# Optimization experiments

Measured on AMD Instinct MI355X. Metric: run time of the kernel, lower is better.

The kernel has to match this reference:

```python
import jax, jax.numpy as jnp
import numpy as np

N_NODES = 100000
N_EDGES = 1600000
D = 128
L = 2


def setup_inputs() -> dict:
    key = jax.random.key(0)
    ks = jax.random.split(key, 8)
    s = 1.0 / np.sqrt(D)
    return {
        "x": jax.random.normal(ks[0], (N_NODES, D), dtype=jnp.float32),
        "edge_index": jax.random.randint(ks[1], (2, N_EDGES), 0, N_NODES, dtype=jnp.int64),
        "edge_weight": jax.random.uniform(ks[2], (N_EDGES,), dtype=jnp.float32),
        "weight": jax.random.normal(ks[3], (L, D, D), dtype=jnp.float32) * s,
        "w_ih": jax.random.normal(ks[4], (3 * D, D), dtype=jnp.float32) * s,
        "w_hh": jax.random.normal(ks[5], (3 * D, D), dtype=jnp.float32) * s,
        "b_ih": jax.random.normal(ks[6], (3 * D,), dtype=jnp.float32) * s,
        "b_hh": jax.random.normal(ks[7], (3 * D,), dtype=jnp.float32) * s,
    }


def _gru_cell(m, h, w_ih, w_hh, b_ih, b_hh):
    # torch.nn.GRUCell: gates ordered (reset, update, new)
    gi = m @ w_ih.T + b_ih  # [N, 3D]
    gh = h @ w_hh.T + b_hh  # [N, 3D]
    i_r, i_z, i_n = jnp.split(gi, 3, axis=-1)
    h_r, h_z, h_n = jnp.split(gh, 3, axis=-1)
    r = jax.nn.sigmoid(i_r + h_r)
    z = jax.nn.sigmoid(i_z + h_z)
    n = jnp.tanh(i_n + r * h_n)
    return (1.0 - z) * n + z * h


def reference(x, edge_index, edge_weight, weight, w_ih, w_hh, b_ih, b_hh):
    src = edge_index[0]
    dst = edge_index[1]
    h = x  # in_channels == out_channels, no zero-padding needed
    for i in range(L):
        m = h @ weight[i]                          # [N, D]
        msg = m[src] * edge_weight[:, None]        # [E, D] gather + scale
        agg = jax.ops.segment_sum(msg, dst, num_segments=N_NODES)  # scatter-add
        h = _gru_cell(agg, h, w_ih, w_hh, b_ih, b_hh)
    return h
```

## Files before the change

kernel.cpp:

```cpp
#include <hip/hip_runtime.h>
#include <hip/hip_bf16.h>
#include <stdint.h>

typedef unsigned short u16;
typedef unsigned long long u64;
typedef __attribute__((ext_vector_type(8))) short bf16x8;
typedef __attribute__((ext_vector_type(4))) float f32x4;

#define DD 128
#define NB 256
#define SB 10240

__device__ __forceinline__ u16 f2bf(float f){
  uint32_t u = __float_as_uint(f);
  uint32_t r = (u + 0x7fffu + ((u >> 16) & 1u)) >> 16;
  return (u16)r;
}
__device__ __forceinline__ float bf2f(u16 h){ return __uint_as_float(((uint32_t)h) << 16); }

struct Frag2 { bf16x8 hi, lo; };

__device__ __forceinline__ Frag2 split8(float4 v0, float4 v1){
  union { float f[8]; uint32_t u[8]; } U;
  *(float4*)&U.f[0] = v0; *(float4*)&U.f[4] = v1;
  union { uint32_t w[4]; bf16x8 v; } H, L;
  #pragma unroll
  for (int q = 0; q < 4; q++){
    uint32_t a = U.u[2*q], b = U.u[2*q+1];
    H.w[q] = __builtin_amdgcn_perm(b, a, 0x07060302);
    float l0 = U.f[2*q]   - __uint_as_float(a & 0xffff0000u);
    float l1 = U.f[2*q+1] - __uint_as_float(b & 0xffff0000u);
    L.w[q] = __builtin_amdgcn_perm(__float_as_uint(l1), __float_as_uint(l0), 0x07060302);
  }
  Frag2 r; r.hi = H.v; r.lo = L.v; return r;
}

__device__ __forceinline__ Frag2 load_afrag_g(const float* A, int row, int k0){
  const float4* p = (const float4*)(A + (size_t)row * DD + k0);
  return split8(p[0], p[1]);
}

__global__ void pack_kernel(const float* __restrict__ whh, const float* __restrict__ bih,
                            const float* __restrict__ bhh, u16* __restrict__ hhb,
                            float* __restrict__ bias, int* __restrict__ gcursor){
  int tid = blockIdx.x * 256 + threadIdx.x;
  int lane = tid & 63;
  int b1 = 6144, b2 = b1 + 512, b3 = b2 + NB;
  if (tid < b1){
    int kc = (tid >> 6) & 3, t = tid >> 8;
    int row = t*16 + (lane & 15), kb = kc*32 + 8*(lane >> 4);
    #pragma unroll
    for (int e = 0; e < 8; e++)
      hhb[(size_t)tid*8 + e] = f2bf(whh[(size_t)row*DD + kb + e]);
  } else if (tid < b2){
    int id = tid - b1;
    if (id < 256)      bias[id] = bih[id] + bhh[id];
    else if (id < 384) bias[id] = bih[id];
    else               bias[id] = bhh[id - 128];
  } else if (tid < b3){
    gcursor[tid - b2] = 0;
  }
}

__global__ __launch_bounds__(256) void wc_kernel(const float* __restrict__ w,
    const float* __restrict__ wih, u16* __restrict__ wcb, int L){
  int tid = blockIdx.x*256 + threadIdx.x;
  if (tid >= L*49152) return;
  int l = tid / 49152;
  int r = tid % 49152;
  int k = r / 384;
  int g = r % 384;
  const float4* wr = (const float4*)(w + (size_t)l*DD*DD + (size_t)k*DD);
  const float4* ir = (const float4*)(wih + (size_t)g*DD);
  float acc = 0.f;
  #pragma unroll
  for (int j = 0; j < 32; j++){
    float4 a = wr[j], b = ir[j];
    acc += a.x*b.x + a.y*b.y + a.z*b.z + a.w*b.w;
  }
  int gate = g >> 7, c = g & 127;
  int jt = c >> 4, lrow = c & 15;
  int kc = k >> 5, sub = (k >> 3) & 3, e = k & 7;
  wcb[(size_t)l*49152 + (size_t)(((gate*8 + jt)*4 + kc)*512 + (sub*16 + lrow)*8 + e)]
      = f2bf(acc);
}

__global__ void conv_kernel(const float* __restrict__ x, u16* __restrict__ hb, int n4){
  int i = blockIdx.x*256 + threadIdx.x;
  if (i < n4){
    float4 v = ((const float4*)x)[i];
    ushort4 o;
    o.x = f2bf(v.x); o.y = f2bf(v.y); o.z = f2bf(v.z); o.w = f2bf(v.w);
    ((ushort4*)hb)[i] = o;
  }
}

__global__ __launch_bounds__(256) void binA_kernel(const int* __restrict__ src,
    const int* __restrict__ dst, const float* __restrict__ ew,
    int* __restrict__ gcursor, u64* __restrict__ staging, int E, int N){
  __shared__ unsigned lcnt[NB];
  __shared__ unsigned lbase[NB];
  __shared__ unsigned lcur[NB];
  __shared__ unsigned gbase[NB];
  __shared__ unsigned char sbucket[4096];
  __shared__ u64 sedge[4096];
  const int CH = 4096;
  int tid = threadIdx.x;
  int e0 = blockIdx.x * CH;

  lcnt[tid] = 0;
  __syncthreads();
  for (int i = tid; i < CH; i += 256){
    int e = e0 + i;
    if (e < E){
      unsigned d = (unsigned)dst[e];
      if (d < (unsigned)N) atomicAdd(&lcnt[d >> 9], 1u);
    }
  }
  __syncthreads();
  lbase[tid] = lcnt[tid];
  __syncthreads();
  for (int off = 1; off < NB; off <<= 1){
    unsigned t = (tid >= off) ? lbase[tid - off] : 0u;
    __syncthreads();
    lbase[tid] += t;
    __syncthreads();
  }
  unsigned total = lbase[NB - 1];
  lbase[tid] -= lcnt[tid];
  gbase[tid] = (unsigned)atomicAdd(&gcursor[tid], (int)lcnt[tid]);
  lcur[tid] = lbase[tid];
  __syncthreads();
  for (int i = tid; i < CH; i += 256){
    int e = e0 + i;
    if (e < E){
      unsigned d = (unsigned)dst[e];
      if (d < (unsigned)N){
        unsigned b = d >> 9;
        unsigned p = atomicAdd(&lcur[b], 1u);
        unsigned s = (unsigned)src[e];
        sedge[p] = ((u64)__float_as_uint(ew[e]) << 32) | ((u64)(s & 0x1FFFFu) << 9)
                 | (u64)(d & 0x1FFu);
        sbucket[p] = (unsigned char)b;
      }
    }
  }
  __syncthreads();
  for (int i = tid; i < (int)total; i += 256){
    unsigned b = sbucket[i];
    unsigned gpos = gbase[b] + ((unsigned)i - lbase[b]);
    if (gpos < SB) staging[(size_t)b*SB + gpos] = sedge[i];
  }
}

__global__ __launch_bounds__(256) void binB_kernel(const u64* __restrict__ staging,
    const int* __restrict__ gcursor, int* __restrict__ row_ptr,
    uint2* __restrict__ entries, int N, int E){
  __shared__ int sg[NB];
  __shared__ unsigned ncnt[512];
  __shared__ unsigned nsc[512];
  __shared__ unsigned ncur[512];
  int tid = threadIdx.x;
  int b = blockIdx.x;
  sg[tid] = gcursor[tid];
  __syncthreads();
  for (int off = 1; off < NB; off <<= 1){
    int t = (tid >= off) ? sg[tid - off] : 0;
    __syncthreads();
    sg[tid] += t;
    __syncthreads();
  }
  int cnt = gcursor[b];
  if (cnt > SB) cnt = SB;
  int base = sg[b] - cnt;
  if (b == NB - 1 && tid == 0) row_ptr[N] = sg[NB - 1];
  const u64* st = staging + (size_t)b * SB;

  ncnt[tid] = 0; ncnt[tid + 256] = 0;
  __syncthreads();
  for (int i = tid; i < cnt; i += 256)
    atomicAdd(&ncnt[(unsigned)(st[i] & 0x1FFu)], 1u);
  __syncthreads();
  nsc[tid] = ncnt[tid]; nsc[tid + 256] = ncnt[tid + 256];
  __syncthreads();
  for (int off = 1; off < 512; off <<= 1){
    unsigned t0 = (tid >= off) ? nsc[tid - off] : 0u;
    unsigned t1 = (tid + 256 >= off) ? nsc[tid + 256 - off] : 0u;
    __syncthreads();
    nsc[tid] += t0; nsc[tid + 256] += t1;
    __syncthreads();
  }
  #pragma unroll
  for (int h = 0; h < 2; h++){
    int k = tid + h*256;
    unsigned excl = nsc[k] - ncnt[k];
    int g = b*512 + k;
    if (g < N) row_ptr[g] = base + (int)excl;
    ncur[k] = excl;
  }
  __syncthreads();
  for (int i = tid; i < cnt; i += 256){
    u64 v = st[i];
    unsigned local = (unsigned)(v & 0x1FFu);
    unsigned p = atomicAdd(&ncur[local], 1u);
    uint2 ent;
    ent.x = (unsigned)((v >> 9) & 0x1FFFFu);
    ent.y = (unsigned)(v >> 32);
    entries[base + p] = ent;
  }
}

__global__ __launch_bounds__(256) void gather_kernel(const int* __restrict__ row_ptr,
    const uint2* __restrict__ entries, const u16* __restrict__ hb,
    float* __restrict__ agg, int N){
  int lane = threadIdx.x & 63;
  int q = lane >> 4;
  int t = lane & 15;
  int node = (blockIdx.x*256 + threadIdx.x) >> 6;
  if (node >= N) return;
  int s = row_ptr[node], e = row_ptr[node + 1];
  float acc[8];
  #pragma unroll
  for (int c = 0; c < 8; c++) acc[c] = 0.f;
  #pragma unroll 4
  for (int i = s; i < e; i += 4){
    int idx = i + q;
    bool valid = idx < e;
    uint2 en = entries[valid ? idx : i];
    float w = valid ? __uint_as_float(en.y) : 0.f;
    uint4 mv = *(const uint4*)(hb + (size_t)en.x*DD + 8*t);
    acc[0] += w * __uint_as_float(mv.x << 16);
    acc[1] += w * __uint_as_float(mv.x & 0xffff0000u);
    acc[2] += w * __uint_as_float(mv.y << 16);
    acc[3] += w * __uint_as_float(mv.y & 0xffff0000u);
    acc[4] += w * __uint_as_float(mv.z << 16);
    acc[5] += w * __uint_as_float(mv.z & 0xffff0000u);
    acc[6] += w * __uint_as_float(mv.w << 16);
    acc[7] += w * __uint_as_float(mv.w & 0xffff0000u);
  }
  #pragma unroll
  for (int c = 0; c < 8; c++){
    acc[c] += __shfl_xor(acc[c], 16);
    acc[c] += __shfl_xor(acc[c], 32);
  }
  if (q == 0){
    float4 o0 = {acc[0], acc[1], acc[2], acc[3]};
    float4 o1 = {acc[4], acc[5], acc[6], acc[7]};
    *(float4*)(agg + (size_t)node*DD + 8*t)     = o0;
    *(float4*)(agg + (size_t)node*DD + 8*t + 4) = o1;
  }
}

__global__ __launch_bounds__(256, 4) void gru_kernel(
    const float* __restrict__ agg, const float* hin,
    const u16* __restrict__ wcb, const u16* __restrict__ hhb,
    const float* __restrict__ bias, float* hout, u16* hbout, int nstripes){
  __shared__ u16 lw[2][12*512];
  int lane = threadIdx.x & 63;
  int wid = threadIdx.x >> 6;
  int stripe = blockIdx.x*4 + wid;
  bool active = stripe < nstripes;
  int n0 = (active ? stripe : (nstripes - 1)) * 16;
  int lrow = lane & 15, lk = lane >> 4;

  Frag2 aa[4], ahf[4];
  #pragma unroll
  for (int kc = 0; kc < 4; kc++){
    int k0 = kc*32 + 8*lk;
    aa[kc]  = load_afrag_g(agg, n0 + lrow, k0);
    ahf[kc] = load_afrag_g(hin, n0 + lrow, k0);
  }

  int q = wid*3;
  int g0 = q >> 2,       kc0 = q & 3;
  int g1 = (q+1) >> 2,   kc1 = (q+1) & 3;
  int g2 = (q+2) >> 2,   kc2 = (q+2) & 3;

  {
    bf16x8 s0 = *(const bf16x8*)(wcb + ((size_t)((g0*8 + 0)*4 + kc0)*64 + lane)*8);
    bf16x8 s1 = *(const bf16x8*)(wcb + ((size_t)((g1*8 + 0)*4 + kc1)*64 + lane)*8);
    bf16x8 s2 = *(const bf16x8*)(wcb + ((size_t)((g2*8 + 0)*4 + kc2)*64 + lane)*8);
    *(bf16x8*)(lw[0] + ((size_t)(q+0)*64 + lane)*8) = s0;
    *(bf16x8*)(lw[0] + ((size_t)(q+1)*64 + lane)*8) = s1;
    *(bf16x8*)(lw[0] + ((size_t)(q+2)*64 + lane)*8) = s2;
  }
  __syncthreads();

  f32x4 zero = {0.f, 0.f, 0.f, 0.f};
  f32x4 ir = zero, iz = zero, in_ = zero, hr = zero, hz = zero, hn = zero;
  for (int ph = 0; ph < 16; ph++){
    int jt = ph >> 1, half = ph & 1;
    bf16x8 n0r, n1r, n2r;
    if (ph < 15){
      int njt = (ph + 1) >> 1;
      const u16* wsrc = ((ph + 1) & 1) ? hhb : wcb;
      n0r = *(const bf16x8*)(wsrc + ((size_t)((g0*8 + njt)*4 + kc0)*64 + lane)*8);
      n1r = *(const bf16x8*)(wsrc + ((size_t)((g1*8 + njt)*4 + kc1)*64 + lane)*8);
      n2r = *(const bf16x8*)(wsrc + ((size_t)((g2*8 + njt)*4 + kc2)*64 + lane)*8);
    }
    const u16* buf = lw[ph & 1];
    if (half == 0){
      ir = zero; iz = zero; in_ = zero;
      #pragma unroll
      for (int kc = 0; kc < 4; kc++){
        bf16x8 b0 = *(const bf16x8*)(buf + ((size_t)(0*4 + kc)*64 + lane)*8);
        bf16x8 b1 = *(const bf16x8*)(buf + ((size_t)(1*4 + kc)*64 + lane)*8);
        bf16x8 b2 = *(const bf16x8*)(buf + ((size_t)(2*4 + kc)*64 + lane)*8);
        ir  = __builtin_amdgcn_mfma_f32_16x16x32_bf16(aa[kc].hi, b0, ir,  0, 0, 0);
        ir  = __builtin_amdgcn_mfma_f32_16x16x32_bf16(aa[kc].lo, b0, ir,  0, 0, 0);
        iz  = __builtin_amdgcn_mfma_f32_16x16x32_bf16(aa[kc].hi, b1, iz,  0, 0, 0);
        iz  = __builtin_amdgcn_mfma_f32_16x16x32_bf16(aa[kc].lo, b1, iz,  0, 0, 0);
        in_ = __builtin_amdgcn_mfma_f32_16x16x32_bf16(aa[kc].hi, b2, in_, 0, 0, 0);
        in_ = __builtin_amdgcn_mfma_f32_16x16x32_bf16(aa[kc].lo, b2, in_, 0, 0, 0);
      }
    } else {
      hr = zero; hz = zero; hn = zero;
      #pragma unroll
      for (int kc = 0; kc < 4; kc++){
        bf16x8 b0 = *(const bf16x8*)(buf + ((size_t)(0*4 + kc)*64 + lane)*8);
        bf16x8 b1 = *(const bf16x8*)(buf + ((size_t)(1*4 + kc)*64 + lane)*8);
        bf16x8 b2 = *(const bf16x8*)(buf + ((size_t)(2*4 + kc)*64 + lane)*8);
        hr = __builtin_amdgcn_mfma_f32_16x16x32_bf16(ahf[kc].hi, b0, hr, 0, 0, 0);
        hr = __builtin_amdgcn_mfma_f32_16x16x32_bf16(ahf[kc].lo, b0, hr, 0, 0, 0);
        hz = __builtin_amdgcn_mfma_f32_16x16x32_bf16(ahf[kc].hi, b1, hz, 0, 0, 0);
        hz = __builtin_amdgcn_mfma_f32_16x16x32_bf16(ahf[kc].lo, b1, hz, 0, 0, 0);
        hn = __builtin_amdgcn_mfma_f32_16x16x32_bf16(ahf[kc].hi, b2, hn, 0, 0, 0);
        hn = __builtin_amdgcn_mfma_f32_16x16x32_bf16(ahf[kc].lo, b2, hn, 0, 0, 0);
      }
      if (active){
        int j = jt*16 + lrow;
        float br = bias[j];
        float bz = bias[128 + j];
        float bi = bias[256 + j];
        float bh = bias[384 + j];
        #pragma unroll
        for (int r = 0; r < 4; r++){
          int node = n0 + lk*4 + r;
          float xr = ir[r] + hr[r] + br;
          float xz = iz[r] + hz[r] + bz;
          float rg = __builtin_amdgcn_rcpf(1.f + __expf(-xr));
          float zg = __builtin_amdgcn_rcpf(1.f + __expf(-xz));
          float xn = in_[r] + bi + rg*(hn[r] + bh);
          xn = fminf(fmaxf(xn, -30.f), 30.f);
          float e2 = __expf(2.f*xn);
          float ng = 1.f - 2.f*__builtin_amdgcn_rcpf(e2 + 1.f);
          float hv = hin[(size_t)node*DD + j];
          float val = ng + zg*(hv - ng);
          hout[(size_t)node*DD + j] = val;
          if (hbout) hbout[(size_t)node*DD + j] = f2bf(val);
        }
      }
    }
    if (ph < 15){
      u16* nbuf = lw[(ph + 1) & 1];
      *(bf16x8*)(nbuf + ((size_t)(q+0)*64 + lane)*8) = n0r;
      *(bf16x8*)(nbuf + ((size_t)(q+1)*64 + lane)*8) = n1r;
      *(bf16x8*)(nbuf + ((size_t)(q+2)*64 + lane)*8) = n2r;
    }
    __syncthreads();
  }
}

extern "C" void kernel_launch(void* const* d_in, const int* in_sizes, int n_in,
                              void* d_out, int out_size, void* d_ws, size_t ws_size,
                              hipStream_t stream){
  const float* x   = (const float*)d_in[0];
  const int*   ei  = (const int*)d_in[1];
  const float* ew  = (const float*)d_in[2];
  const float* wgt = (const float*)d_in[3];
  const float* wih = (const float*)d_in[4];
  const float* whh = (const float*)d_in[5];
  const float* bih = (const float*)d_in[6];
  const float* bhh = (const float*)d_in[7];
  float* out = (float*)d_out;

  const int N = in_sizes[0] / DD;
  const int E = in_sizes[2];
  const int L = in_sizes[3] / (DD * DD);

  char* p = (char*)d_ws;
  auto alloc = [&](size_t b) -> char* {
    char* r = p; p += (b + 255) & ~(size_t)255; return r;
  };
  u16*   wcb     = (u16*)  alloc((size_t)L * 49152 * 2);
  u16*   hhb     = (u16*)  alloc((size_t)6144 * 8 * 2);
  float* bias    = (float*)alloc(512 * 4);
  int*   gcursor = (int*)  alloc(NB * 4);
  int*   row_ptr = (int*)  alloc(((size_t)N + 1) * 4);
  uint2* entries = (uint2*)alloc((size_t)E * 8);
  u16*   hb      = (u16*)  alloc((size_t)N * DD * 2);
  float* agg     = (float*)alloc((size_t)N * DD * 4);
  u64*   staging = (u64*)agg;

  const int* src = ei;
  const int* dst = ei + E;

  int packN = 6144 + 512 + NB;
  pack_kernel<<<(packN + 255)/256, 256, 0, stream>>>(whh, bih, bhh, hhb, bias, gcursor);
  wc_kernel<<<(L*49152 + 255)/256, 256, 0, stream>>>(wgt, wih, wcb, L);
  conv_kernel<<<(N*DD/4 + 255)/256, 256, 0, stream>>>(x, hb, N*DD/4);
  binA_kernel<<<(E + 4095)/4096, 256, 0, stream>>>(src, dst, ew, gcursor, staging, E, N);
  binB_kernel<<<NB, 256, 0, stream>>>(staging, gcursor, row_ptr, entries, N, E);

  int nstripes = N / 16;
  int ggrid = (nstripes + 3) / 4;
  for (int l = 0; l < L; l++){
    const float* hin = (l == 0) ? x : out;
    gather_kernel<<<(N*64 + 255)/256, 256, 0, stream>>>(row_ptr, entries, hb, agg, N);
    gru_kernel<<<ggrid, 256, 0, stream>>>(agg, hin, wcb + (size_t)l*49152, hhb, bias,
                                          out, (l == L - 1) ? nullptr : hb, nstripes);
  }
}
```

Baseline: 333.7 us.

## Restructure GRU kernel with register-resident weights and split-bf16 node state

The GRU kernel becomes persistent: 256 blocks of 512 threads loop over 16-node stripes. Each wave owns one 16-column output tile and keeps all its input-side and hidden-side bf16 weight fragments in registers, which removes the LDS double-buffered weight streaming and its 16 barrier phases. The aggregation and hidden state are now stored as hi/lo bf16 pairs in global memory, written by the gather and conv kernels, instead of being split from fp32 inside the GRU kernel. Risks are high register pressure from the resident weights under launch_bounds(512,2), which could cause spills, and lower occupancy for a kernel that is mostly loading activations; the hidden state is also updated in place.

```diff
diff --git a/kernel.cpp b/kernel.cpp
--- a/kernel.cpp
+++ b/kernel.cpp
@@ -17,28 +17,6 @@
   return (u16)r;
 }
 __device__ __forceinline__ float bf2f(u16 h){ return __uint_as_float(((uint32_t)h) << 16); }
-
-struct Frag2 { bf16x8 hi, lo; };
-
-__device__ __forceinline__ Frag2 split8(float4 v0, float4 v1){
-  union { float f[8]; uint32_t u[8]; } U;
-  *(float4*)&U.f[0] = v0; *(float4*)&U.f[4] = v1;
-  union { uint32_t w[4]; bf16x8 v; } H, L;
-  #pragma unroll
-  for (int q = 0; q < 4; q++){
-    uint32_t a = U.u[2*q], b = U.u[2*q+1];
-    H.w[q] = __builtin_amdgcn_perm(b, a, 0x07060302);
-    float l0 = U.f[2*q]   - __uint_as_float(a & 0xffff0000u);
-    float l1 = U.f[2*q+1] - __uint_as_float(b & 0xffff0000u);
-    L.w[q] = __builtin_amdgcn_perm(__float_as_uint(l1), __float_as_uint(l0), 0x07060302);
-  }
-  Frag2 r; r.hi = H.v; r.lo = L.v; return r;
-}
-
-__device__ __forceinline__ Frag2 load_afrag_g(const float* A, int row, int k0){
-  const float4* p = (const float4*)(A + (size_t)row * DD + k0);
-  return split8(p[0], p[1]);
-}
 
 __global__ void pack_kernel(const float* __restrict__ whh, const float* __restrict__ bih,
                             const float* __restrict__ bhh, u16* __restrict__ hhb,
@@ -85,13 +63,23 @@
       = f2bf(acc);
 }
 
-__global__ void conv_kernel(const float* __restrict__ x, u16* __restrict__ hb, int n4){
+__global__ void conv_kernel(const float* __restrict__ x, u16* __restrict__ hbH,
+                            u16* __restrict__ hbL, int n4){
   int i = blockIdx.x*256 + threadIdx.x;
   if (i < n4){
     float4 v = ((const float4*)x)[i];
-    ushort4 o;
-    o.x = f2bf(v.x); o.y = f2bf(v.y); o.z = f2bf(v.z); o.w = f2bf(v.w);
-    ((ushort4*)hb)[i] = o;
+    ushort4 oh, ol;
+    float f[4] = {v.x, v.y, v.z, v.w};
+    u16 h[4], l[4];
+    #pragma unroll
+    for (int e = 0; e < 4; e++){
+      h[e] = f2bf(f[e]);
+      l[e] = f2bf(f[e] - bf2f(h[e]));
+    }
+    oh.x = h[0]; oh.y = h[1]; oh.z = h[2]; oh.w = h[3];
+    ol.x = l[0]; ol.y = l[1]; ol.z = l[2]; ol.w = l[3];
+    ((ushort4*)hbH)[i] = oh;
+    ((ushort4*)hbL)[i] = ol;
   }
 }
 
@@ -211,8 +199,8 @@
 }
 
 __global__ __launch_bounds__(256) void gather_kernel(const int* __restrict__ row_ptr,
-    const uint2* __restrict__ entries, const u16* __restrict__ hb,
-    float* __restrict__ agg, int N){
+    const uint2* __restrict__ entries, const u16* __restrict__ hbH,
+    u16* __restrict__ aggH, u16* __restrict__ aggL, int N){
   int lane = threadIdx.x & 63;
   int q = lane >> 4;
   int t = lane & 15;
@@ -228,7 +216,7 @@
     bool valid = idx < e;
     uint2 en = entries[valid ? idx : i];
     float w = valid ? __uint_as_float(en.y) : 0.f;
-    uint4 mv = *(const uint4*)(hb + (size_t)en.x*DD + 8*t);
+    uint4 mv = *(const uint4*)(hbH + (size_t)en.x*DD + 8*t);
     acc[0] += w * __uint_as_float(mv.x << 16);
     acc[1] += w * __uint_as_float(mv.x & 0xffff0000u);
     acc[2] += w * __uint_as_float(mv.y << 16);
@@ -244,120 +232,102 @@
     acc[c] += __shfl_xor(acc[c], 32);
   }
   if (q == 0){
-    float4 o0 = {acc[0], acc[1], acc[2], acc[3]};
-    float4 o1 = {acc[4], acc[5], acc[6], acc[7]};
-    *(float4*)(agg + (size_t)node*DD + 8*t)     = o0;
-    *(float4*)(agg + (size_t)node*DD + 8*t + 4) = o1;
-  }
-}
-
-__global__ __launch_bounds__(256, 4) void gru_kernel(
-    const float* __restrict__ agg, const float* hin,
+    uint32_t hw[4], lw[4];
+    #pragma unroll
+    for (int c = 0; c < 4; c++){
+      u16 h0 = f2bf(acc[2*c]), h1 = f2bf(acc[2*c+1]);
+      u16 l0 = f2bf(acc[2*c]   - bf2f(h0));
+      u16 l1 = f2bf(acc[2*c+1] - bf2f(h1));
+      hw[c] = (uint32_t)h0 | ((uint32_t)h1 << 16);
+      lw[c] = (uint32_t)l0 | ((uint32_t)l1 << 16);
+    }
+    uint4 oh = {hw[0], hw[1], hw[2], hw[3]};
+    uint4 ol = {lw[0], lw[1], lw[2], lw[3]};
+    *(uint4*)(aggH + (size_t)node*DD + 8*t) = oh;
+    *(uint4*)(aggL + (size_t)node*DD + 8*t) = ol;
+  }
+}
+
+__global__ __launch_bounds__(512, 2) void gru_kernel(
+    const u16* __restrict__ aggH, const u16* __restrict__ aggL,
+    u16* hbH, u16* hbL,
     const u16* __restrict__ wcb, const u16* __restrict__ hhb,
-    const float* __restrict__ bias, float* hout, u16* hbout, int nstripes){
-  __shared__ u16 lw[2][12*512];
+    const float* __restrict__ bias, float* __restrict__ out,
+    int final_, int nstripes){
   int lane = threadIdx.x & 63;
-  int wid = threadIdx.x >> 6;
-  int stripe = blockIdx.x*4 + wid;
-  bool active = stripe < nstripes;
-  int n0 = (active ? stripe : (nstripes - 1)) * 16;
+  int jt = threadIdx.x >> 6;
   int lrow = lane & 15, lk = lane >> 4;
-
-  Frag2 aa[4], ahf[4];
-  #pragma unroll
-  for (int kc = 0; kc < 4; kc++){
-    int k0 = kc*32 + 8*lk;
-    aa[kc]  = load_afrag_g(agg, n0 + lrow, k0);
-    ahf[kc] = load_afrag_g(hin, n0 + lrow, k0);
-  }
-
-  int q = wid*3;
-  int g0 = q >> 2,       kc0 = q & 3;
-  int g1 = (q+1) >> 2,   kc1 = (q+1) & 3;
-  int g2 = (q+2) >> 2,   kc2 = (q+2) & 3;
-
-  {
-    bf16x8 s0 = *(const bf16x8*)(wcb + ((size_t)((g0*8 + 0)*4 + kc0)*64 + lane)*8);
-    bf16x8 s1 = *(const bf16x8*)(wcb + ((size_t)((g1*8 + 0)*4 + kc1)*64 + lane)*8);
-    bf16x8 s2 = *(const bf16x8*)(wcb + ((size_t)((g2*8 + 0)*4 + kc2)*64 + lane)*8);
-    *(bf16x8*)(lw[0] + ((size_t)(q+0)*64 + lane)*8) = s0;
-    *(bf16x8*)(lw[0] + ((size_t)(q+1)*64 + lane)*8) = s1;
-    *(bf16x8*)(lw[0] + ((size_t)(q+2)*64 + lane)*8) = s2;
-  }
-  __syncthreads();
+  int j = jt*16 + lrow;
+
+  bf16x8 wI[3][4], wH[3][4];
+  #pragma unroll
+  for (int g = 0; g < 3; g++){
+    #pragma unroll
+    for (int kc = 0; kc < 4; kc++){
+      wI[g][kc] = *(const bf16x8*)(wcb + ((size_t)((g*8 + jt)*4 + kc)*64 + lane)*8);
+      wH[g][kc] = *(const bf16x8*)(hhb + ((size_t)((g*8 + jt)*4 + kc)*64 + lane)*8);
+    }
+  }
+  float br = bias[j], bz = bias[128 + j], bi = bias[256 + j], bh = bias[384 + j];
 
   f32x4 zero = {0.f, 0.f, 0.f, 0.f};
-  f32x4 ir = zero, iz = zero, in_ = zero, hr = zero, hz = zero, hn = zero;
-  for (int ph = 0; ph < 16; ph++){
-    int jt = ph >> 1, half = ph & 1;
-    bf16x8 n0r, n1r, n2r;
-    if (ph < 15){
-      int njt = (ph + 1) >> 1;
-      const u16* wsrc = ((ph + 1) & 1) ? hhb : wcb;
-      n0r = *(const bf16x8*)(wsrc + ((size_t)((g0*8 + njt)*4 + kc0)*64 + lane)*8);
-      n1r = *(const bf16x8*)(wsrc + ((size_t)((g1*8 + njt)*4 + kc1)*64 + lane)*8);
-      n2r = *(const bf16x8*)(wsrc + ((size_t)((g2*8 + njt)*4 + kc2)*64 + lane)*8);
-    }
-    const u16* buf = lw[ph & 1];
-    if (half == 0){
-      ir = zero; iz = zero; in_ = zero;
-      #pragma unroll
-      for (int kc = 0; kc < 4; kc++){
-        bf16x8 b0 = *(const bf16x8*)(buf + ((size_t)(0*4 + kc)*64 + lane)*8);
-        bf16x8 b1 = *(const bf16x8*)(buf + ((size_t)(1*4 + kc)*64 + lane)*8);
-        bf16x8 b2 = *(const bf16x8*)(buf + ((size_t)(2*4 + kc)*64 + lane)*8);
-        ir  = __builtin_amdgcn_mfma_f32_16x16x32_bf16(aa[kc].hi, b0, ir,  0, 0, 0);
-        ir  = __builtin_amdgcn_mfma_f32_16x16x32_bf16(aa[kc].lo, b0, ir,  0, 0, 0);
-        iz  = __builtin_amdgcn_mfma_f32_16x16x32_bf16(aa[kc].hi, b1, iz,  0, 0, 0);
-        iz  = __builtin_amdgcn_mfma_f32_16x16x32_bf16(aa[kc].lo, b1, iz,  0, 0, 0);
-        in_ = __builtin_amdgcn_mfma_f32_16x16x32_bf16(aa[kc].hi, b2, in_, 0, 0, 0);
-        in_ = __builtin_amdgcn_mfma_f32_16x16x32_bf16(aa[kc].lo, b2, in_, 0, 0, 0);
+  for (int s = blockIdx.x; s < nstripes; s += gridDim.x){
+    int n0 = s*16;
+    bf16x8 aH[4], aL[4], hHf[4], hLf[4];
+    #pragma unroll
+    for (int kc = 0; kc < 4; kc++){
+      size_t o = (size_t)(n0 + lrow)*DD + kc*32 + 8*lk;
+      aH[kc]  = *(const bf16x8*)(aggH + o);
+      aL[kc]  = *(const bf16x8*)(aggL + o);
+      hHf[kc] = *(const bf16x8*)(hbH + o);
+      hLf[kc] = *(const bf16x8*)(hbL + o);
+    }
+    u16 vh[4], vl[4];
+    #pragma unroll
+    for (int r = 0; r < 4; r++){
+      size_t o = (size_t)(n0 + lk*4 + r)*DD + j;
+      vh[r] = hbH[o];
+      vl[r] = hbL[o];
+    }
+    __syncthreads();
+
+    f32x4 ir = zero, iz = zero, in_ = zero, hr = zero, hz = zero, hn = zero;
+    #pragma unroll
+    for (int kc = 0; kc < 4; kc++){
+      ir  = __builtin_amdgcn_mfma_f32_16x16x32_bf16(aH[kc],  wI[0][kc], ir,  0, 0, 0);
+      ir  = __builtin_amdgcn_mfma_f32_16x16x32_bf16(aL[kc],  wI[0][kc], ir,  0, 0, 0);
+      iz  = __builtin_amdgcn_mfma_f32_16x16x32_bf16(aH[kc],  wI[1][kc], iz,  0, 0, 0);
+      iz  = __builtin_amdgcn_mfma_f32_16x16x32_bf16(aL[kc],  wI[1][kc], iz,  0, 0, 0);
+      in_ = __builtin_amdgcn_mfma_f32_16x16x32_bf16(aH[kc],  wI[2][kc], in_, 0, 0, 0);
+      in_ = __builtin_amdgcn_mfma_f32_16x16x32_bf16(aL[kc],  wI[2][kc], in_, 0, 0, 0);
+      hr  = __builtin_amdgcn_mfma_f32_16x16x32_bf16(hHf[kc], wH[0][kc], hr,  0, 0, 0);
+      hr  = __builtin_amdgcn_mfma_f32_16x16x32_bf16(hLf[kc], wH[0][kc], hr,  0, 0, 0);
+      hz  = __builtin_amdgcn_mfma_f32_16x16x32_bf16(hHf[kc], wH[1][kc], hz,  0, 0, 0);
+      hz  = __builtin_amdgcn_mfma_f32_16x16x32_bf16(hLf[kc], wH[1][kc], hz,  0, 0, 0);
+      hn  = __builtin_amdgcn_mfma_f32_16x16x32_bf16(hHf[kc], wH[2][kc], hn,  0, 0, 0);
+      hn  = __builtin_amdgcn_mfma_f32_16x16x32_bf16(hLf[kc], wH[2][kc], hn,  0, 0, 0);
+    }
+    #pragma unroll
+    for (int r = 0; r < 4; r++){
+      float xr = ir[r] + hr[r] + br;
+      float xz = iz[r] + hz[r] + bz;
+      float rg = __builtin_amdgcn_rcpf(1.f + __expf(-xr));
+      float zg = __builtin_amdgcn_rcpf(1.f + __expf(-xz));
+      float xn = in_[r] + bi + rg*(hn[r] + bh);
+      xn = fminf(fmaxf(xn, -30.f), 30.f);
+      float e2 = __expf(2.f*xn);
+      float ng = 1.f - 2.f*__builtin_amdgcn_rcpf(e2 + 1.f);
+      float hv = bf2f(vh[r]) + bf2f(vl[r]);
+      float val = ng + zg*(hv - ng);
+      size_t o = (size_t)(n0 + lk*4 + r)*DD + j;
+      if (final_){
+        out[o] = val;
+      } else {
+        u16 hi = f2bf(val);
+        hbH[o] = hi;
+        hbL[o] = f2bf(val - bf2f(hi));
       }
-    } else {
-      hr = zero; hz = zero; hn = zero;
-      #pragma unroll
-      for (int kc = 0; kc < 4; kc++){
-        bf16x8 b0 = *(const bf16x8*)(buf + ((size_t)(0*4 + kc)*64 + lane)*8);
-        bf16x8 b1 = *(const bf16x8*)(buf + ((size_t)(1*4 + kc)*64 + lane)*8);
-        bf16x8 b2 = *(const bf16x8*)(buf + ((size_t)(2*4 + kc)*64 + lane)*8);
-        hr = __builtin_amdgcn_mfma_f32_16x16x32_bf16(ahf[kc].hi, b0, hr, 0, 0, 0);
-        hr = __builtin_amdgcn_mfma_f32_16x16x32_bf16(ahf[kc].lo, b0, hr, 0, 0, 0);
-        hz = __builtin_amdgcn_mfma_f32_16x16x32_bf16(ahf[kc].hi, b1, hz, 0, 0, 0);
-        hz = __builtin_amdgcn_mfma_f32_16x16x32_bf16(ahf[kc].lo, b1, hz, 0, 0, 0);
-        hn = __builtin_amdgcn_mfma_f32_16x16x32_bf16(ahf[kc].hi, b2, hn, 0, 0, 0);
-        hn = __builtin_amdgcn_mfma_f32_16x16x32_bf16(ahf[kc].lo, b2, hn, 0, 0, 0);
-      }
-      if (active){
-        int j = jt*16 + lrow;
-        float br = bias[j];
-        float bz = bias[128 + j];
-        float bi = bias[256 + j];
-        float bh = bias[384 + j];
-        #pragma unroll
-        for (int r = 0; r < 4; r++){
-          int node = n0 + lk*4 + r;
-          float xr = ir[r] + hr[r] + br;
-          float xz = iz[r] + hz[r] + bz;
-          float rg = __builtin_amdgcn_rcpf(1.f + __expf(-xr));
-          float zg = __builtin_amdgcn_rcpf(1.f + __expf(-xz));
-          float xn = in_[r] + bi + rg*(hn[r] + bh);
-          xn = fminf(fmaxf(xn, -30.f), 30.f);
-          float e2 = __expf(2.f*xn);
-          float ng = 1.f - 2.f*__builtin_amdgcn_rcpf(e2 + 1.f);
-          float hv = hin[(size_t)node*DD + j];
-          float val = ng + zg*(hv - ng);
-          hout[(size_t)node*DD + j] = val;
-          if (hbout) hbout[(size_t)node*DD + j] = f2bf(val);
-        }
-      }
-    }
-    if (ph < 15){
-      u16* nbuf = lw[(ph + 1) & 1];
-      *(bf16x8*)(nbuf + ((size_t)(q+0)*64 + lane)*8) = n0r;
-      *(bf16x8*)(nbuf + ((size_t)(q+1)*64 + lane)*8) = n1r;
-      *(bf16x8*)(nbuf + ((size_t)(q+2)*64 + lane)*8) = n2r;
-    }
-    __syncthreads();
+    }
   }
 }
 
@@ -388,9 +358,11 @@
   int*   gcursor = (int*)  alloc(NB * 4);
   int*   row_ptr = (int*)  alloc(((size_t)N + 1) * 4);
   uint2* entries = (uint2*)alloc((size_t)E * 8);
-  u16*   hb      = (u16*)  alloc((size_t)N * DD * 2);
-  float* agg     = (float*)alloc((size_t)N * DD * 4);
-  u64*   staging = (u64*)agg;
+  u16*   hbH     = (u16*)  alloc((size_t)N * DD * 2);
+  u16*   hbL     = (u16*)  alloc((size_t)N * DD * 2);
+  u16*   aggH    = (u16*)  alloc((size_t)N * DD * 2);
+  u16*   aggL    = (u16*)  alloc((size_t)N * DD * 2);
+  u64*   staging = (u64*)aggH;
 
   const int* src = ei;
   const int* dst = ei + E;
@@ -398,16 +370,16 @@
   int packN = 6144 + 512 + NB;
   pack_kernel<<<(packN + 255)/256, 256, 0, stream>>>(whh, bih, bhh, hhb, bias, gcursor);
   wc_kernel<<<(L*49152 + 255)/256, 256, 0, stream>>>(wgt, wih, wcb, L);
-  conv_kernel<<<(N*DD/4 + 255)/256, 256, 0, stream>>>(x, hb, N*DD/4);
+  conv_kernel<<<(N*DD/4 + 255)/256, 256, 0, stream>>>(x, hbH, hbL, N*DD/4);
   binA_kernel<<<(E + 4095)/4096, 256, 0, stream>>>(src, dst, ew, gcursor, staging, E, N);
   binB_kernel<<<NB, 256, 0, stream>>>(staging, gcursor, row_ptr, entries, N, E);
 
   int nstripes = N / 16;
-  int ggrid = (nstripes + 3) / 4;
   for (int l = 0; l < L; l++){
-    const float* hin = (l == 0) ? x : out;
-    gather_kernel<<<(N*64 + 255)/256, 256, 0, stream>>>(row_ptr, entries, hb, agg, N);
-    gru_kernel<<<ggrid, 256, 0, stream>>>(agg, hin, wcb + (size_t)l*49152, hhb, bias,
-                                          out, (l == L - 1) ? nullptr : hb, nstripes);
-  }
-}
+    gather_kernel<<<(N*64 + 255)/256, 256, 0, stream>>>(row_ptr, entries, hbH,
+                                                        aggH, aggL, N);
+    gru_kernel<<<256, 512, 0, stream>>>(aggH, aggL, hbH, hbL,
+                                        wcb + (size_t)l*49152, hhb, bias,
+                                        out, (l == L - 1) ? 1 : 0, nstripes);
+  }
+}
```

Result: slower. 450.1 us (+34.9%).

## Widen GRU blocks to 8 waves and stage both weight halves per tile

Applied to the files above, without the earlier changes.

The GRU kernel now uses 512-thread blocks with 8 waves. Each wave stages 3 of the 24 weight fragments, so the input and hidden weight slices for one output column tile are loaded into shared memory together. The 16 phases become 8 iterations, each running all six gate MFMA chains, which halves the number of block barriers and lets the gate math follow each tile directly. In exchange the block uses twice as much LDS and has more waves waiting at each barrier, which may reduce occupancy.

```diff
diff --git a/kernel.cpp b/kernel.cpp
--- a/kernel.cpp
+++ b/kernel.cpp
@@ -251,14 +251,14 @@
   }
 }
 
-__global__ __launch_bounds__(256, 4) void gru_kernel(
+__global__ __launch_bounds__(512, 4) void gru_kernel(
     const float* __restrict__ agg, const float* hin,
     const u16* __restrict__ wcb, const u16* __restrict__ hhb,
     const float* __restrict__ bias, float* hout, u16* hbout, int nstripes){
-  __shared__ u16 lw[2][12*512];
+  __shared__ u16 lw[2][24*512];
   int lane = threadIdx.x & 63;
   int wid = threadIdx.x >> 6;
-  int stripe = blockIdx.x*4 + wid;
+  int stripe = blockIdx.x*8 + wid;
   bool active = stripe < nstripes;
   int n0 = (active ? stripe : (nstripes - 1)) * 16;
   int lrow = lane & 15, lk = lane >> 4;
@@ -277,9 +277,15 @@
   int g2 = (q+2) >> 2,   kc2 = (q+2) & 3;
 
   {
-    bf16x8 s0 = *(const bf16x8*)(wcb + ((size_t)((g0*8 + 0)*4 + kc0)*64 + lane)*8);
-    bf16x8 s1 = *(const bf16x8*)(wcb + ((size_t)((g1*8 + 0)*4 + kc1)*64 + lane)*8);
-    bf16x8 s2 = *(const bf16x8*)(wcb + ((size_t)((g2*8 + 0)*4 + kc2)*64 + lane)*8);
+    const u16* s0p = (g0 < 3) ? (wcb + ((size_t)((g0*8 + 0)*4 + kc0)*64 + lane)*8)
+                              : (hhb + ((size_t)(((g0-3)*8 + 0)*4 + kc0)*64 + lane)*8);
+    const u16* s1p = (g1 < 3) ? (wcb + ((size_t)((g1*8 + 0)*4 + kc1)*64 + lane)*8)
+                              : (hhb + ((size_t)(((g1-3)*8 + 0)*4 + kc1)*64 + lane)*8);
+    const u16* s2p = (g2 < 3) ? (wcb + ((size_t)((g2*8 + 0)*4 + kc2)*64 + lane)*8)
+                              : (hhb + ((size_t)(((g2-3)*8 + 0)*4 + kc2)*64 + lane)*8);
+    bf16x8 s0 = *(const bf16x8*)s0p;
+    bf16x8 s1 = *(const bf16x8*)s1p;
+    bf16x8 s2 = *(const bf16x8*)s2p;
     *(bf16x8*)(lw[0] + ((size_t)(q+0)*64 + lane)*8) = s0;
     *(bf16x8*)(lw[0] + ((size_t)(q+1)*64 + lane)*8) = s1;
     *(bf16x8*)(lw[0] + ((size_t)(q+2)*64 + lane)*8) = s2;
@@ -287,72 +293,68 @@
   __syncthreads();
 
   f32x4 zero = {0.f, 0.f, 0.f, 0.f};
-  f32x4 ir = zero, iz = zero, in_ = zero, hr = zero, hz = zero, hn = zero;
-  for (int ph = 0; ph < 16; ph++){
-    int jt = ph >> 1, half = ph & 1;
+  for (int jt = 0; jt < 8; jt++){
     bf16x8 n0r, n1r, n2r;
-    if (ph < 15){
-      int njt = (ph + 1) >> 1;
-      const u16* wsrc = ((ph + 1) & 1) ? hhb : wcb;
-      n0r = *(const bf16x8*)(wsrc + ((size_t)((g0*8 + njt)*4 + kc0)*64 + lane)*8);
-      n1r = *(const bf16x8*)(wsrc + ((size_t)((g1*8 + njt)*4 + kc1)*64 + lane)*8);
-      n2r = *(const bf16x8*)(wsrc + ((size_t)((g2*8 + njt)*4 + kc2)*64 + lane)*8);
-    }
-    const u16* buf = lw[ph & 1];
-    if (half == 0){
-      ir = zero; iz = zero; in_ = zero;
+    if (jt < 7){
+      int nj = jt + 1;
+      const u16* s0p = (g0 < 3) ? (wcb + ((size_t)((g0*8 + nj)*4 + kc0)*64 + lane)*8)
+                                : (hhb + ((size_t)(((g0-3)*8 + nj)*4 + kc0)*64 + lane)*8);
+      const u16* s1p = (g1 < 3) ? (wcb + ((size_t)((g1*8 + nj)*4 + kc1)*64 + lane)*8)
+                                : (hhb + ((size_t)(((g1-3)*8 + nj)*4 + kc1)*64 + lane)*8);
+      const u16* s2p = (g2 < 3) ? (wcb + ((size_t)((g2*8 + nj)*4 + kc2)*64 + lane)*8)
+                                : (hhb + ((size_t)(((g2-3)*8 + nj)*4 + kc2)*64 + lane)*8);
+      n0r = *(const bf16x8*)s0p;
+      n1r = *(const bf16x8*)s1p;
+      n2r = *(const bf16x8*)s2p;
+    }
+    const u16* buf = lw[jt & 1];
+    f32x4 ir = zero, iz = zero, in_ = zero, hr = zero, hz = zero, hn = zero;
+    #pragma unroll
+    for (int kc = 0; kc < 4; kc++){
+      bf16x8 b0 = *(const bf16x8*)(buf + ((size_t)(0*4 + kc)*64 + lane)*8);
+      bf16x8 b1 = *(const bf16x8*)(buf + ((size_t)(1*4 + kc)*64 + lane)*8);
+      bf16x8 b2 = *(const bf16x8*)(buf + ((size_t)(2*4 + kc)*64 + lane)*8);
+      bf16x8 b3 = *(const bf16x8*)(buf + ((size_t)(3*4 + kc)*64 + lane)*8);
+      bf16x8 b4 = *(const bf16x8*)(buf + ((size_t)(4*4 + kc)*64 + lane)*8);
+      bf16x8 b5 = *(const bf16x8*)(buf + ((size_t)(5*4 + kc)*64 + lane)*8);
+      ir  = __builtin_amdgcn_mfma_f32_16x16x32_bf16(aa[kc].hi,  b0, ir,  0, 0, 0);
+      ir  = __builtin_amdgcn_mfma_f32_16x16x32_bf16(aa[kc].lo,  b0, ir,  0, 0, 0);
+      iz  = __builtin_amdgcn_mfma_f32_16x16x32_bf16(aa[kc].hi,  b1, iz,  0, 0, 0);
+      iz  = __builtin_amdgcn_mfma_f32_16x16x32_bf16(aa[kc].lo,  b1, iz,  0, 0, 0);
+      in_ = __builtin_amdgcn_mfma_f32_16x16x32_bf16(aa[kc].hi,  b2, in_, 0, 0, 0);
+      in_ = __builtin_amdgcn_mfma_f32_16x16x32_bf16(aa[kc].lo,  b2, in_, 0, 0, 0);
+      hr  = __builtin_amdgcn_mfma_f32_16x16x32_bf16(ahf[kc].hi, b3, hr,  0, 0, 0);
+      hr  = __builtin_amdgcn_mfma_f32_16x16x32_bf16(ahf[kc].lo, b3, hr,  0, 0, 0);
+      hz  = __builtin_amdgcn_mfma_f32_16x16x32_bf16(ahf[kc].hi, b4, hz,  0, 0, 0);
+      hz  = __builtin_amdgcn_mfma_f32_16x16x32_bf16(ahf[kc].lo, b4, hz,  0, 0, 0);
+      hn  = __builtin_amdgcn_mfma_f32_16x16x32_bf16(ahf[kc].hi, b5, hn,  0, 0, 0);
+      hn  = __builtin_amdgcn_mfma_f32_16x16x32_bf16(ahf[kc].lo, b5, hn,  0, 0, 0);
+    }
+    if (active){
+      int j = jt*16 + lrow;
+      float br = bias[j];
+      float bz = bias[128 + j];
+      float bi = bias[256 + j];
+      float bh = bias[384 + j];
       #pragma unroll
-      for (int kc = 0; kc < 4; kc++){
-        bf16x8 b0 = *(const bf16x8*)(buf + ((size_t)(0*4 + kc)*64 + lane)*8);
-        bf16x8 b1 = *(const bf16x8*)(buf + ((size_t)(1*4 + kc)*64 + lane)*8);
-        bf16x8 b2 = *(const bf16x8*)(buf + ((size_t)(2*4 + kc)*64 + lane)*8);
-        ir  = __builtin_amdgcn_mfma_f32_16x16x32_bf16(aa[kc].hi, b0, ir,  0, 0, 0);
-        ir  = __builtin_amdgcn_mfma_f32_16x16x32_bf16(aa[kc].lo, b0, ir,  0, 0, 0);
-        iz  = __builtin_amdgcn_mfma_f32_16x16x32_bf16(aa[kc].hi, b1, iz,  0, 0, 0);
-        iz  = __builtin_amdgcn_mfma_f32_16x16x32_bf16(aa[kc].lo, b1, iz,  0, 0, 0);
-        in_ = __builtin_amdgcn_mfma_f32_16x16x32_bf16(aa[kc].hi, b2, in_, 0, 0, 0);
-        in_ = __builtin_amdgcn_mfma_f32_16x16x32_bf16(aa[kc].lo, b2, in_, 0, 0, 0);
+      for (int r = 0; r < 4; r++){
+        int node = n0 + lk*4 + r;
+        float xr = ir[r] + hr[r] + br;
+        float xz = iz[r] + hz[r] + bz;
+        float rg = __builtin_amdgcn_rcpf(1.f + __expf(-xr));
+        float zg = __builtin_amdgcn_rcpf(1.f + __expf(-xz));
+        float xn = in_[r] + bi + rg*(hn[r] + bh);
+        xn = fminf(fmaxf(xn, -30.f), 30.f);
+        float e2 = __expf(2.f*xn);
+        float ng = 1.f - 2.f*__builtin_amdgcn_rcpf(e2 + 1.f);
+        float hv = hin[(size_t)node*DD + j];
+        float val = ng + zg*(hv - ng);
+        hout[(size_t)node*DD + j] = val;
+        if (hbout) hbout[(size_t)node*DD + j] = f2bf(val);
       }
-    } else {
-      hr = zero; hz = zero; hn = zero;
-      #pragma unroll
-      for (int kc = 0; kc < 4; kc++){
-        bf16x8 b0 = *(const bf16x8*)(buf + ((size_t)(0*4 + kc)*64 + lane)*8);
-        bf16x8 b1 = *(const bf16x8*)(buf + ((size_t)(1*4 + kc)*64 + lane)*8);
-        bf16x8 b2 = *(const bf16x8*)(buf + ((size_t)(2*4 + kc)*64 + lane)*8);
-        hr = __builtin_amdgcn_mfma_f32_16x16x32_bf16(ahf[kc].hi, b0, hr, 0, 0, 0);
-        hr = __builtin_amdgcn_mfma_f32_16x16x32_bf16(ahf[kc].lo, b0, hr, 0, 0, 0);
-        hz = __builtin_amdgcn_mfma_f32_16x16x32_bf16(ahf[kc].hi, b1, hz, 0, 0, 0);
-        hz = __builtin_amdgcn_mfma_f32_16x16x32_bf16(ahf[kc].lo, b1, hz, 0, 0, 0);
-        hn = __builtin_amdgcn_mfma_f32_16x16x32_bf16(ahf[kc].hi, b2, hn, 0, 0, 0);
-        hn = __builtin_amdgcn_mfma_f32_16x16x32_bf16(ahf[kc].lo, b2, hn, 0, 0, 0);
-      }
-      if (active){
-        int j = jt*16 + lrow;
-        float br = bias[j];
-        float bz = bias[128 + j];
-        float bi = bias[256 + j];
-        float bh = bias[384 + j];
-        #pragma unroll
-        for (int r = 0; r < 4; r++){
-          int node = n0 + lk*4 + r;
-          float xr = ir[r] + hr[r] + br;
-          float xz = iz[r] + hz[r] + bz;
-          float rg = __builtin_amdgcn_rcpf(1.f + __expf(-xr));
-          float zg = __builtin_amdgcn_rcpf(1.f + __expf(-xz));
-          float xn = in_[r] + bi + rg*(hn[r] + bh);
-          xn = fminf(fmaxf(xn, -30.f), 30.f);
-          float e2 = __expf(2.f*xn);
-          float ng = 1.f - 2.f*__builtin_amdgcn_rcpf(e2 + 1.f);
-          float hv = hin[(size_t)node*DD + j];
-          float val = ng + zg*(hv - ng);
-          hout[(size_t)node*DD + j] = val;
-          if (hbout) hbout[(size_t)node*DD + j] = f2bf(val);
-        }
-      }
-    }
-    if (ph < 15){
-      u16* nbuf = lw[(ph + 1) & 1];
+    }
+    if (jt < 7){
+      u16* nbuf = lw[(jt + 1) & 1];
       *(bf16x8*)(nbuf + ((size_t)(q+0)*64 + lane)*8) = n0r;
       *(bf16x8*)(nbuf + ((size_t)(q+1)*64 + lane)*8) = n1r;
       *(bf16x8*)(nbuf + ((size_t)(q+2)*64 + lane)*8) = n2r;
@@ -403,11 +405,11 @@
   binB_kernel<<<NB, 256, 0, stream>>>(staging, gcursor, row_ptr, entries, N, E);
 
   int nstripes = N / 16;
-  int ggrid = (nstripes + 3) / 4;
+  int ggrid8 = (nstripes + 7) / 8;
   for (int l = 0; l < L; l++){
     const float* hin = (l == 0) ? x : out;
     gather_kernel<<<(N*64 + 255)/256, 256, 0, stream>>>(row_ptr, entries, hb, agg, N);
-    gru_kernel<<<ggrid, 256, 0, stream>>>(agg, hin, wcb + (size_t)l*49152, hhb, bias,
-                                          out, (l == L - 1) ? nullptr : hb, nstripes);
-  }
-}
+    gru_kernel<<<ggrid8, 512, 0, stream>>>(agg, hin, wcb + (size_t)l*49152, hhb, bias,
+                                           out, (l == L - 1) ? nullptr : hb, nstripes);
+  }
+}
```

Result: slower. 385.3 us (+15.5%).
